# Kernel tuning notes

Measured on AMD Instinct MI355X. Metric: run time of the kernel, lower is better.

Reference implementation:

```python
import jax, jax.numpy as jnp
import numpy as np

B, W, H = 16384, 16, 16
NUM_CLASSES = 1024
EMBED = 4
OUT = 1024

def setup_inputs() -> dict:
    key = jax.random.key(0)
    k0, k1, k2 = jax.random.split(key, 3)
    x = jax.random.randint(k0, (B, W, H), 0, NUM_CLASSES, dtype=jnp.int32)
    W_embed = jax.random.normal(k1, (NUM_CLASSES, EMBED), dtype=jnp.float32) * 0.02
    b_embed = jnp.zeros((EMBED,), dtype=jnp.float32)
    W_dense = jax.random.normal(k2, (EMBED * W * H, OUT), dtype=jnp.float32) * 0.02
    b_dense = jnp.zeros((OUT,), dtype=jnp.float32)
    return {"x": x, "W_embed": W_embed, "b_embed": b_embed, "W_dense": W_dense, "b_dense": b_dense}

def reference(x, W_embed, b_embed, W_dense, b_dense):
    # one_hot(x, C) @ W_embed + b_embed is mathematically a row-gather of W_embed
    emb = W_embed[x] + b_embed                 # (B, W, H, EMBED)
    flat = emb.reshape(emb.shape[0], -1)        # (B, W*H*EMBED)  == rearrange '... w h c -> ... (w h c)'
    return flat @ W_dense + b_dense             # (B, OUT)
```

## Files before the change

kernel.cpp:

```cpp
#include <hip/hip_runtime.h>
#include <stdint.h>
#include <stddef.h>

typedef __attribute__((ext_vector_type(8))) short bf16x8;
typedef __attribute__((ext_vector_type(4))) short bf16x4;
typedef __attribute__((ext_vector_type(4))) float f32x4;

typedef const __attribute__((address_space(1))) void* gptr1_t;
typedef __attribute__((address_space(3))) void* lptr3_t;

#define GLOAD_LDS16(gp, lp) \
  __builtin_amdgcn_global_load_lds((gptr1_t)(gp), (lptr3_t)(lp), 16, 0, 0)

__device__ __forceinline__ uint16_t f2bf(float f) {
  uint32_t u = __builtin_bit_cast(uint32_t, f);
  u += 0x7fffu + ((u >> 16) & 1u);
  return (uint16_t)(u >> 16);
}

#define MB   16384
#define NP   256
#define KDIM 1024
#define NDIM 1024
#define NCLS 1024

#define BM  128
#define BN  128
#define BKH 32
#define BK  64
#define NK  (KDIM / BK)

__global__ void build_bt_kernel(const float* __restrict__ Wd,
                                uint16_t* __restrict__ Bt) {
  __shared__ uint16_t tile[32][33];
  const int k0 = blockIdx.y * 32;
  const int n0 = blockIdx.x * 32;
  const int tx = threadIdx.x;
  const int ty = threadIdx.y;
  #pragma unroll
  for (int r = 0; r < 32; r += 8)
    tile[ty + r][tx] = f2bf(Wd[(size_t)(k0 + ty + r) * NDIM + n0 + tx]);
  __syncthreads();
  #pragma unroll
  for (int r = 0; r < 32; r += 8)
    Bt[(size_t)(n0 + ty + r) * KDIM + k0 + tx] = tile[tx][ty + r];
}

__global__ __launch_bounds__(256) void fused_gemm_kernel(
    const int* __restrict__ x,
    const float* __restrict__ We,
    const float* __restrict__ be,
    const uint16_t* __restrict__ Bt,
    const float* __restrict__ bias,
    float* __restrict__ C) {
  __shared__ __align__(16) uint16_t web[NCLS * 4];
  __shared__ __align__(16) uint16_t As[2][BM * BKH];
  __shared__ __align__(16) uint16_t Bs[2][BN * BKH];

  const int tid  = threadIdx.x;
  const int bm   = blockIdx.x;
  const int bn   = blockIdx.y;
  const int wave = tid >> 6;
  const int lane = tid & 63;
  const int wr   = wave >> 1;
  const int wc   = wave & 1;
  const int lm   = lane & 15;
  const int q    = lane >> 4;

  const int row0 = bm * BM;
  const int col0 = bn * BN;

  {
    const float4 bb = *(const float4*)be;
    #pragma unroll
    for (int c0 = 0; c0 < NCLS; c0 += 256) {
      const int c = c0 + tid;
      const float4 w = *(const float4*)(We + (size_t)c * 4);
      bf16x4 t;
      t[0] = (short)f2bf(w.x + bb.x);
      t[1] = (short)f2bf(w.y + bb.y);
      t[2] = (short)f2bf(w.z + bb.z);
      t[3] = (short)f2bf(w.w + bb.w);
      *(bf16x4*)(web + (size_t)c * 4) = t;
    }
  }

  const int srow = tid >> 2;
  const int scol = (tid & 3) * 8;
  const int arow = tid >> 2;
  const int apos = (tid & 3) * 4;
  const int ah   = apos >> 3;
  const int aoff = (apos & 7) * 4;

  f32x4 acc[4][4];
  #pragma unroll
  for (int i = 0; i < 4; i++)
    #pragma unroll
    for (int j = 0; j < 4; j++)
      acc[i][j] = (f32x4){0.f, 0.f, 0.f, 0.f};

  const int* xr_a = x + (size_t)(row0      + arow) * NP + apos;
  const int* xr_b = x + (size_t)(row0 + 64 + arow) * NP + apos;

  int4 xqa = *(const int4*)xr_a;
  int4 xqb = *(const int4*)xr_b;

  __syncthreads();

  for (int kt = 0; kt < NK; ++kt) {
    const int k0 = kt * BK;
    #pragma unroll
    for (int h = 0; h < 2; ++h) {
      GLOAD_LDS16(Bt + (size_t)(col0      + srow) * KDIM + k0 + h * BKH + scol, Bs[h] + tid * 8);
      GLOAD_LDS16(Bt + (size_t)(col0 + 64 + srow) * KDIM + k0 + h * BKH + scol, Bs[h] + 2048 + tid * 8);
    }

    {
      uint16_t* da = As[ah] + arow * BKH + aoff;
      uint16_t* db = As[ah] + (64 + arow) * BKH + aoff;
      union { bf16x8 v; struct { bf16x4 lo, hi; } s; } u;
      u.s.lo = *(const bf16x4*)(web + ((unsigned)xqa.x * 4u));
      u.s.hi = *(const bf16x4*)(web + ((unsigned)xqa.y * 4u));
      *(bf16x8*)(da) = u.v;
      u.s.lo = *(const bf16x4*)(web + ((unsigned)xqa.z * 4u));
      u.s.hi = *(const bf16x4*)(web + ((unsigned)xqa.w * 4u));
      *(bf16x8*)(da + 8) = u.v;
      u.s.lo = *(const bf16x4*)(web + ((unsigned)xqb.x * 4u));
      u.s.hi = *(const bf16x4*)(web + ((unsigned)xqb.y * 4u));
      *(bf16x8*)(db) = u.v;
      u.s.lo = *(const bf16x4*)(web + ((unsigned)xqb.z * 4u));
      u.s.hi = *(const bf16x4*)(web + ((unsigned)xqb.w * 4u));
      *(bf16x8*)(db + 8) = u.v;
    }

    if (kt + 1 < NK) {
      xqa = *(const int4*)(xr_a + (kt + 1) * 16);
      xqb = *(const int4*)(xr_b + (kt + 1) * 16);
    }

    __syncthreads();

    #pragma unroll
    for (int h = 0; h < 2; ++h) {
      bf16x8 af[4], bfr[4];
      #pragma unroll
      for (int i = 0; i < 4; i++)
        af[i] = *(const bf16x8*)(As[h] + (wr * 64 + i * 16 + lm) * BKH + q * 8);
      #pragma unroll
      for (int j = 0; j < 4; j++)
        bfr[j] = *(const bf16x8*)(Bs[h] + (wc * 64 + j * 16 + lm) * BKH + q * 8);

      #pragma unroll
      for (int i = 0; i < 4; i++)
        #pragma unroll
        for (int j = 0; j < 4; j++)
          acc[i][j] = __builtin_amdgcn_mfma_f32_16x16x32_bf16(af[i], bfr[j], acc[i][j], 0, 0, 0);
    }

    __syncthreads();
  }

  float bvals[4];
  #pragma unroll
  for (int j = 0; j < 4; j++)
    bvals[j] = bias[col0 + wc * 64 + j * 16 + lm];

  #pragma unroll
  for (int i = 0; i < 4; i++) {
    const int rbase = row0 + wr * 64 + i * 16 + q * 4;
    #pragma unroll
    for (int j = 0; j < 4; j++) {
      const int col = col0 + wc * 64 + j * 16 + lm;
      #pragma unroll
      for (int r = 0; r < 4; r++)
        C[(size_t)(rbase + r) * NDIM + col] = acc[i][j][r] + bvals[j];
    }
  }
}

__global__ void naive_kernel(const int* __restrict__ x,
                             const float* __restrict__ We,
                             const float* __restrict__ be,
                             const float* __restrict__ Wd,
                             const float* __restrict__ bd,
                             float* __restrict__ out) {
  __shared__ float emb[KDIM];
  const int b = blockIdx.x;
  const int tid = threadIdx.x;
  {
    const int cls = x[(size_t)b * NP + tid];
    const float4 e  = *(const float4*)(We + (size_t)cls * 4);
    const float4 bb = *(const float4*)be;
    emb[tid * 4 + 0] = e.x + bb.x;
    emb[tid * 4 + 1] = e.y + bb.y;
    emb[tid * 4 + 2] = e.z + bb.z;
    emb[tid * 4 + 3] = e.w + bb.w;
  }
  __syncthreads();
  float acc0 = bd[tid], acc1 = bd[tid + 256], acc2 = bd[tid + 512], acc3 = bd[tid + 768];
  for (int k = 0; k < KDIM; ++k) {
    const float a = emb[k];
    const float* w = Wd + (size_t)k * NDIM + tid;
    acc0 += a * w[0];
    acc1 += a * w[256];
    acc2 += a * w[512];
    acc3 += a * w[768];
  }
  float* o = out + (size_t)b * NDIM + tid;
  o[0] = acc0; o[256] = acc1; o[512] = acc2; o[768] = acc3;
}

extern "C" void kernel_launch(void* const* d_in, const int* in_sizes, int n_in,
                              void* d_out, int out_size, void* d_ws, size_t ws_size,
                              hipStream_t stream) {
  const int*   x  = (const int*)d_in[0];
  const float* We = (const float*)d_in[1];
  const float* be = (const float*)d_in[2];
  const float* Wd = (const float*)d_in[3];
  const float* bd = (const float*)d_in[4];
  float* out = (float*)d_out;

  const size_t needB = (size_t)NDIM * KDIM * sizeof(uint16_t);

  if (ws_size >= needB) {
    uint16_t* Btw = (uint16_t*)d_ws;
    build_bt_kernel<<<dim3(NDIM / 32, KDIM / 32), dim3(32, 8), 0, stream>>>(Wd, Btw);
    fused_gemm_kernel<<<dim3(MB / BM, NDIM / BN), 256, 0, stream>>>(x, We, be, Btw, bd, out);
  } else {
    naive_kernel<<<MB, 256, 0, stream>>>(x, We, be, Wd, bd, out);
  }
}
```

Before: 131.4 us.

## Pre-swizzle B into MFMA fragment order and match A LDS layout

The B-transpose kernel now writes the bf16 weight matrix in a tiled layout where each (column block, k-tile, half) chunk is contiguous and laid out in MFMA fragment order (group, quad, lane, element). The GEMM then copies B into LDS with fully contiguous 16-byte global loads, and both A and B fragment reads from LDS become one contiguous lane-indexed 16-byte read per lane, which should reduce LDS bank conflicts and global access scatter. The A gather writes into the same fragment-ordered layout. The next-x prefetch is also moved after the barrier.

```diff
diff --git a/kernel.cpp b/kernel.cpp
--- a/kernel.cpp
+++ b/kernel.cpp
@@ -26,12 +26,12 @@
 
 #define BM  128
 #define BN  128
-#define BKH 32
 #define BK  64
 #define NK  (KDIM / BK)
 
+
 __global__ void build_bt_kernel(const float* __restrict__ Wd,
-                                uint16_t* __restrict__ Bt) {
+                                uint16_t* __restrict__ Btf) {
   __shared__ uint16_t tile[32][33];
   const int k0 = blockIdx.y * 32;
   const int n0 = blockIdx.x * 32;
@@ -42,20 +42,26 @@
     tile[ty + r][tx] = f2bf(Wd[(size_t)(k0 + ty + r) * NDIM + n0 + tx]);
   __syncthreads();
   #pragma unroll
-  for (int r = 0; r < 32; r += 8)
-    Bt[(size_t)(n0 + ty + r) * KDIM + k0 + tx] = tile[tx][ty + r];
+  for (int r = 0; r < 32; r += 8) {
+    const int n = n0 + ty + r;
+    const int k = k0 + tx;
+    const int bn = n >> 7, g = (n >> 4) & 7, m = n & 15;
+    const int kt = k >> 6, h = (k >> 5) & 1, q = (k >> 3) & 3, e = k & 7;
+    Btf[(size_t)((bn * 16 + kt) * 2 + h) * 4096 + (size_t)(g * 64 + q * 16 + m) * 8 + e]
+        = tile[tx][ty + r];
+  }
 }
 
 __global__ __launch_bounds__(256) void fused_gemm_kernel(
     const int* __restrict__ x,
     const float* __restrict__ We,
     const float* __restrict__ be,
-    const uint16_t* __restrict__ Bt,
+    const uint16_t* __restrict__ Btf,
     const float* __restrict__ bias,
     float* __restrict__ C) {
   __shared__ __align__(16) uint16_t web[NCLS * 4];
-  __shared__ __align__(16) uint16_t As[2][BM * BKH];
-  __shared__ __align__(16) uint16_t Bs[2][BN * BKH];
+  __shared__ __align__(16) uint16_t As[2][4096];
+  __shared__ __align__(16) uint16_t Bs[2][4096];
 
   const int tid  = threadIdx.x;
   const int bm   = blockIdx.x;
@@ -85,12 +91,14 @@
     }
   }
 
-  const int srow = tid >> 2;
-  const int scol = (tid & 3) * 8;
   const int arow = tid >> 2;
   const int apos = (tid & 3) * 4;
-  const int ah   = apos >> 3;
-  const int aoff = (apos & 7) * 4;
+  const int ah   = (tid >> 1) & 1;
+  const int aq0  = (tid & 1) * 2;
+  const int ag   = arow >> 4;
+  const int am   = arow & 15;
+  uint16_t* const da = As[ah] + (size_t)((ag    ) * 64 + aq0 * 16 + am) * 8;
+  uint16_t* const db = As[ah] + (size_t)((ag + 4) * 64 + aq0 * 16 + am) * 8;
 
   f32x4 acc[4][4];
   #pragma unroll
@@ -105,50 +113,50 @@
   int4 xqa = *(const int4*)xr_a;
   int4 xqb = *(const int4*)xr_b;
 
+  const uint16_t* const btb = Btf + (size_t)bn * (NK * 2 * 4096);
+
   __syncthreads();
 
   for (int kt = 0; kt < NK; ++kt) {
-    const int k0 = kt * BK;
+    const uint16_t* bsrc = btb + (size_t)kt * 2 * 4096;
     #pragma unroll
     for (int h = 0; h < 2; ++h) {
-      GLOAD_LDS16(Bt + (size_t)(col0      + srow) * KDIM + k0 + h * BKH + scol, Bs[h] + tid * 8);
-      GLOAD_LDS16(Bt + (size_t)(col0 + 64 + srow) * KDIM + k0 + h * BKH + scol, Bs[h] + 2048 + tid * 8);
+      GLOAD_LDS16(bsrc + (size_t)h * 4096 +        tid * 8, Bs[h] + tid * 8);
+      GLOAD_LDS16(bsrc + (size_t)h * 4096 + 2048 + tid * 8, Bs[h] + 2048 + tid * 8);
     }
 
     {
-      uint16_t* da = As[ah] + arow * BKH + aoff;
-      uint16_t* db = As[ah] + (64 + arow) * BKH + aoff;
       union { bf16x8 v; struct { bf16x4 lo, hi; } s; } u;
       u.s.lo = *(const bf16x4*)(web + ((unsigned)xqa.x * 4u));
       u.s.hi = *(const bf16x4*)(web + ((unsigned)xqa.y * 4u));
       *(bf16x8*)(da) = u.v;
       u.s.lo = *(const bf16x4*)(web + ((unsigned)xqa.z * 4u));
       u.s.hi = *(const bf16x4*)(web + ((unsigned)xqa.w * 4u));
-      *(bf16x8*)(da + 8) = u.v;
+      *(bf16x8*)(da + 128) = u.v;
       u.s.lo = *(const bf16x4*)(web + ((unsigned)xqb.x * 4u));
       u.s.hi = *(const bf16x4*)(web + ((unsigned)xqb.y * 4u));
       *(bf16x8*)(db) = u.v;
       u.s.lo = *(const bf16x4*)(web + ((unsigned)xqb.z * 4u));
       u.s.hi = *(const bf16x4*)(web + ((unsigned)xqb.w * 4u));
-      *(bf16x8*)(db + 8) = u.v;
-    }
+      *(bf16x8*)(db + 128) = u.v;
+    }
+
+    __syncthreads();
 
     if (kt + 1 < NK) {
       xqa = *(const int4*)(xr_a + (kt + 1) * 16);
       xqb = *(const int4*)(xr_b + (kt + 1) * 16);
     }
 
-    __syncthreads();
-
     #pragma unroll
     for (int h = 0; h < 2; ++h) {
       bf16x8 af[4], bfr[4];
       #pragma unroll
       for (int i = 0; i < 4; i++)
-        af[i] = *(const bf16x8*)(As[h] + (wr * 64 + i * 16 + lm) * BKH + q * 8);
+        af[i] = *(const bf16x8*)(As[h] + (size_t)((wr * 4 + i) * 64 + lane) * 8);
       #pragma unroll
       for (int j = 0; j < 4; j++)
-        bfr[j] = *(const bf16x8*)(Bs[h] + (wc * 64 + j * 16 + lm) * BKH + q * 8);
+        bfr[j] = *(const bf16x8*)(Bs[h] + (size_t)((wc * 4 + j) * 64 + lane) * 8);
 
       #pragma unroll
       for (int i = 0; i < 4; i++)
```

Result: slower. 134.0 us (+2.0%).
